# Kernel optimization log

Measured on AMD Instinct MI355X. Metric: run time of the kernel, lower is better.

The kernel has to match this reference:

```python
import jax, jax.numpy as jnp
import numpy as np

B, F0, F1, E, C = 256, 39, 39, 16, 1  # batch, feature_nums[0], feature_nums[1], emb_size, w_channels
_ROWS, _COLS = np.tril_indices(F1, k=-1)  # strict lower triangle of (F1, F0); row-major order matches masked_select
I = _ROWS.shape[0]  # interaction_num = 741
BN_EPS = 1e-5


def setup_inputs() -> dict:
    key = jax.random.key(0)
    k1, k2, k3 = jax.random.split(key, 3)
    xi = jax.random.normal(k1, (B, F0, E), dtype=jnp.float32)
    xj = jax.random.normal(k2, (B, F1, E), dtype=jnp.float32)
    # W param is (1,1,C,E,E) in torch; keep the broadcastable core (C,E,E). Xavier-uniform bound.
    bound = float(np.sqrt(6.0 / (E + E)))
    W = jax.random.uniform(k3, (C, E, E), dtype=jnp.float32, minval=-bound, maxval=bound)
    gamma = jnp.ones((I,), dtype=jnp.float32)   # BatchNorm2d weight
    beta = jnp.zeros((I,), dtype=jnp.float32)   # BatchNorm2d bias
    return {"xi": xi, "xj": xj, "W": W, "gamma": gamma, "beta": beta}


def reference(xi, xj, W, gamma, beta):
    rows = jnp.asarray(_ROWS)
    cols = jnp.asarray(_COLS)
    # raw_cross[b,f1,f0,e1,e2] = xj[b,f1,e1] * xi[b,f0,e2]; only keep strict-lower-tri (f1,f0) pairs.
    # Compute triangular pairs directly instead of materializing the full (B,F1,F0,E,E) tensor.
    cross = xj[:, rows, :, None] * xi[:, cols, None, :]  # (B, I, E, E)
    # BatchNorm2d (training-mode batch stats, biased variance) over channels I
    mean = jnp.mean(cross, axis=(0, 2, 3), keepdims=True)            # (1, I, 1, 1)
    var = jnp.mean(jnp.square(cross - mean), axis=(0, 2, 3), keepdims=True)
    normed = (cross - mean) * jax.lax.rsqrt(var + BN_EPS)
    normed = normed * gamma[None, :, None, None] + beta[None, :, None, None]
    # broadcast multiply with W over w_channels, then transpose(1,2)
    out = normed[:, :, None, :, :] * W[None, None, :, :, :]          # (B, I, C, E, E)
    return jnp.transpose(out, (0, 2, 1, 3, 4))                        # (B, C, I, E, E)
```

## Files before the change

kernel.cpp:

```cpp
#include <hip/hip_runtime.h>
#include <math.h>

#define BB 256
#define FF 39
#define EE 16
#define II 741
#define BN_EPS 1e-5f

typedef float vfloat4 __attribute__((ext_vector_type(4)));


__global__ __launch_bounds__(256) void
stats_kernel(const float* __restrict__ xi,
             const float* __restrict__ xj,
             const float* __restrict__ gamma,
             const float* __restrict__ beta,
             float* __restrict__ ws) {
    int wid = (blockIdx.x * blockDim.x + threadIdx.x) >> 6;
    int lane = threadIdx.x & 63;
    if (wid >= II) return;
    int i = wid;
    int r = (int)((1.0f + sqrtf(8.0f * (float)i + 1.0f)) * 0.5f);
    while (r * (r - 1) / 2 > i) --r;
    while ((r + 1) * r / 2 <= i) ++r;
    int c = i - r * (r - 1) / 2;

    float sumS = 0.f, sumQ = 0.f;
#pragma unroll
    for (int b = lane; b < BB; b += 64) {
        const vfloat4* xjr = reinterpret_cast<const vfloat4*>(xj + (b * FF + r) * EE);
        const vfloat4* xic = reinterpret_cast<const vfloat4*>(xi + (b * FF + c) * EE);
        float sj = 0.f, qj = 0.f, si = 0.f, qi = 0.f;
#pragma unroll
        for (int k = 0; k < 4; ++k) {
            vfloat4 vj = xjr[k];
            vfloat4 vi = xic[k];
            sj += vj.x + vj.y + vj.z + vj.w;
            qj += vj.x * vj.x + vj.y * vj.y + vj.z * vj.z + vj.w * vj.w;
            si += vi.x + vi.y + vi.z + vi.w;
            qi += vi.x * vi.x + vi.y * vi.y + vi.z * vi.z + vi.w * vi.w;
        }
        sumS += sj * si;
        sumQ += qj * qi;
    }
#pragma unroll
    for (int off = 32; off > 0; off >>= 1) {
        sumS += __shfl_xor(sumS, off);
        sumQ += __shfl_xor(sumQ, off);
    }
    if (lane == 0) {
        const float invN = 1.0f / (float)(BB * EE * EE);
        float mean = sumS * invN;
        float ex2 = sumQ * invN;
        float var = ex2 - mean * mean;
        float inv_std = 1.0f / sqrtf(var + BN_EPS);
        float a = gamma[i] * inv_std;
        float d = beta[i] - mean * a;
        vfloat4 e;
        e.x = a; e.y = d; e.z = (float)(r * EE); e.w = (float)(c * EE);
        reinterpret_cast<vfloat4*>(ws)[i] = e;
    }
}

#define CPW 8
__global__ __launch_bounds__(256) void
cross_bn_kernel(const float* __restrict__ xi,
                const float* __restrict__ xj,
                const float* __restrict__ W,
                const float* __restrict__ ws,
                float* __restrict__ out) {
    const vfloat4* T = reinterpret_cast<const vfloat4*>(ws);

    int b = blockIdx.y;
    int t = threadIdx.x;
    int l = t & 63;
    int e1 = l >> 2;
    int e2q = l & 3;
    int wv = t >> 6;

    vfloat4 w4 = reinterpret_cast<const vfloat4*>(W)[e1 * 4 + e2q];

    const float* xib = xi + b * FF * EE;
    const float* xjb = xj + b * FF * EE;
    float* outb = out + (size_t)b * II * EE * EE;

    int ibase = blockIdx.x * (4 * CPW) + wv * CPW;

    if (ibase + CPW <= II) {
        vfloat4 tb[CPW];
#pragma unroll
        for (int k = 0; k < CPW; ++k) tb[k] = T[ibase + k];
        float xjs[CPW];
        vfloat4 xi4[CPW];
#pragma unroll
        for (int k = 0; k < CPW; ++k) {
            xjs[k] = xjb[(int)tb[k].z + e1];
            xi4[k] = reinterpret_cast<const vfloat4*>(xib + (int)tb[k].w)[e2q];
        }
#pragma unroll
        for (int k = 0; k < CPW; ++k) {
            vfloat4 o;
            o.x = (xjs[k] * xi4[k].x * tb[k].x + tb[k].y) * w4.x;
            o.y = (xjs[k] * xi4[k].y * tb[k].x + tb[k].y) * w4.y;
            o.z = (xjs[k] * xi4[k].z * tb[k].x + tb[k].y) * w4.z;
            o.w = (xjs[k] * xi4[k].w * tb[k].x + tb[k].y) * w4.w;
            vfloat4* dst = reinterpret_cast<vfloat4*>(outb + (size_t)(ibase + k) * (EE * EE)) + l;
            *dst = o;
        }
    } else {
#pragma unroll
        for (int k = 0; k < CPW; ++k) {
            int i = ibase + k;
            if (i >= II) break;
            vfloat4 tb = T[i];
            float xjs = xjb[(int)tb.z + e1];
            vfloat4 xi4 = reinterpret_cast<const vfloat4*>(xib + (int)tb.w)[e2q];
            vfloat4 o;
            o.x = (xjs * xi4.x * tb.x + tb.y) * w4.x;
            o.y = (xjs * xi4.y * tb.x + tb.y) * w4.y;
            o.z = (xjs * xi4.z * tb.x + tb.y) * w4.z;
            o.w = (xjs * xi4.w * tb.x + tb.y) * w4.w;
            vfloat4* dst = reinterpret_cast<vfloat4*>(outb + (size_t)i * (EE * EE)) + l;
            *dst = o;
        }
    }
}

extern "C" void kernel_launch(void* const* d_in, const int* in_sizes, int n_in,
                              void* d_out, int out_size, void* d_ws, size_t ws_size,
                              hipStream_t stream) {
    const float* xi = (const float*)d_in[0];
    const float* xj = (const float*)d_in[1];
    const float* W = (const float*)d_in[2];
    const float* gamma = (const float*)d_in[3];
    const float* beta = (const float*)d_in[4];
    float* out = (float*)d_out;
    float* ws = (float*)d_ws;

    stats_kernel<<<dim3((II * 64 + 255) / 256), 256, 0, stream>>>(xi, xj, gamma, beta, ws);
    const int CPB = 4 * CPW;
    cross_bn_kernel<<<dim3((II + CPB - 1) / CPB, BB), 256, 0, stream>>>(xi, xj, W, ws, out);
}
```

Measured before the change: 45.28 us.

## Process several batches per block and use constant offset table

Each block of the main kernel now handles four batch rows, so the per-channel scale/shift and offsets are loaded once and reused across those rows, and the grid shrinks by four. The (row, col) index decode moves to a compile-time constant-memory table of packed offsets, which also lets the stats kernel skip its sqrt-based index recovery and shrinks the workspace entries to two floats. Fewer blocks means less parallelism and more sequential stores per wave on a kernel that is mostly bound by output writes.

Result: faster. 43.14 us (-4.7%).

```diff
diff --git a/kernel.cpp b/kernel.cpp
--- a/kernel.cpp
+++ b/kernel.cpp
@@ -6,8 +6,24 @@
 #define EE 16
 #define II 741
 #define BN_EPS 1e-5f
+#define CPW 8
+#define NB 4
 
 typedef float vfloat4 __attribute__((ext_vector_type(4)));
+typedef float vfloat2 __attribute__((ext_vector_type(2)));
+
+struct OffTab { unsigned int v[II]; };
+static constexpr OffTab make_off() {
+    OffTab t{};
+    int i = 0;
+    for (int r = 1; r < FF; ++r)
+        for (int c = 0; c < r; ++c) {
+            t.v[i] = ((unsigned)(r * EE) << 16) | (unsigned)(c * EE);
+            ++i;
+        }
+    return t;
+}
+__constant__ OffTab g_off = make_off();
 
 
 __global__ __launch_bounds__(256) void
@@ -20,16 +36,15 @@
     int lane = threadIdx.x & 63;
     if (wid >= II) return;
     int i = wid;
-    int r = (int)((1.0f + sqrtf(8.0f * (float)i + 1.0f)) * 0.5f);
-    while (r * (r - 1) / 2 > i) --r;
-    while ((r + 1) * r / 2 <= i) ++r;
-    int c = i - r * (r - 1) / 2;
+    unsigned o = g_off.v[i];
+    int joff = (int)(o >> 16);
+    int coff = (int)(o & 0xffffu);
 
     float sumS = 0.f, sumQ = 0.f;
 #pragma unroll
     for (int b = lane; b < BB; b += 64) {
-        const vfloat4* xjr = reinterpret_cast<const vfloat4*>(xj + (b * FF + r) * EE);
-        const vfloat4* xic = reinterpret_cast<const vfloat4*>(xi + (b * FF + c) * EE);
+        const vfloat4* xjr = reinterpret_cast<const vfloat4*>(xj + b * FF * EE + joff);
+        const vfloat4* xic = reinterpret_cast<const vfloat4*>(xi + b * FF * EE + coff);
         float sj = 0.f, qj = 0.f, si = 0.f, qi = 0.f;
 #pragma unroll
         for (int k = 0; k < 4; ++k) {
@@ -56,22 +71,20 @@
         float inv_std = 1.0f / sqrtf(var + BN_EPS);
         float a = gamma[i] * inv_std;
         float d = beta[i] - mean * a;
-        vfloat4 e;
-        e.x = a; e.y = d; e.z = (float)(r * EE); e.w = (float)(c * EE);
-        reinterpret_cast<vfloat4*>(ws)[i] = e;
+        vfloat2 e;
+        e.x = a; e.y = d;
+        reinterpret_cast<vfloat2*>(ws)[i] = e;
     }
 }
 
-#define CPW 8
 __global__ __launch_bounds__(256) void
 cross_bn_kernel(const float* __restrict__ xi,
                 const float* __restrict__ xj,
                 const float* __restrict__ W,
                 const float* __restrict__ ws,
                 float* __restrict__ out) {
-    const vfloat4* T = reinterpret_cast<const vfloat4*>(ws);
+    const vfloat2* T2 = reinterpret_cast<const vfloat2*>(ws);
 
-    int b = blockIdx.y;
     int t = threadIdx.x;
     int l = t & 63;
     int e1 = l >> 2;
@@ -80,48 +93,66 @@
 
     vfloat4 w4 = reinterpret_cast<const vfloat4*>(W)[e1 * 4 + e2q];
 
-    const float* xib = xi + b * FF * EE;
-    const float* xjb = xj + b * FF * EE;
-    float* outb = out + (size_t)b * II * EE * EE;
-
-    int ibase = blockIdx.x * (4 * CPW) + wv * CPW;
+    int ibase = __builtin_amdgcn_readfirstlane(blockIdx.x * (4 * CPW) + wv * CPW);
+    int b0 = blockIdx.y * NB;
 
     if (ibase + CPW <= II) {
-        vfloat4 tb[CPW];
-#pragma unroll
-        for (int k = 0; k < CPW; ++k) tb[k] = T[ibase + k];
-        float xjs[CPW];
-        vfloat4 xi4[CPW];
+        int joff[CPW], coff[CPW];
+        float a[CPW], d[CPW];
 #pragma unroll
         for (int k = 0; k < CPW; ++k) {
-            xjs[k] = xjb[(int)tb[k].z + e1];
-            xi4[k] = reinterpret_cast<const vfloat4*>(xib + (int)tb[k].w)[e2q];
+            unsigned o = g_off.v[ibase + k];
+            joff[k] = (int)(o >> 16);
+            coff[k] = (int)(o & 0xffffu);
+            vfloat2 ad = T2[ibase + k];
+            a[k] = ad.x; d[k] = ad.y;
         }
 #pragma unroll
-        for (int k = 0; k < CPW; ++k) {
-            vfloat4 o;
-            o.x = (xjs[k] * xi4[k].x * tb[k].x + tb[k].y) * w4.x;
-            o.y = (xjs[k] * xi4[k].y * tb[k].x + tb[k].y) * w4.y;
-            o.z = (xjs[k] * xi4[k].z * tb[k].x + tb[k].y) * w4.z;
-            o.w = (xjs[k] * xi4[k].w * tb[k].x + tb[k].y) * w4.w;
-            vfloat4* dst = reinterpret_cast<vfloat4*>(outb + (size_t)(ibase + k) * (EE * EE)) + l;
-            *dst = o;
+        for (int bb = 0; bb < NB; ++bb) {
+            int b = b0 + bb;
+            const float* xib = xi + b * FF * EE;
+            const float* xjb = xj + b * FF * EE;
+            float* outb = out + (size_t)b * (II * EE * EE) + (size_t)ibase * (EE * EE);
+            float xjs[CPW];
+            vfloat4 xi4[CPW];
+#pragma unroll
+            for (int k = 0; k < CPW; ++k) {
+                xjs[k] = xjb[joff[k] + e1];
+                xi4[k] = reinterpret_cast<const vfloat4*>(xib + coff[k])[e2q];
+            }
+#pragma unroll
+            for (int k = 0; k < CPW; ++k) {
+                vfloat4 o4;
+                o4.x = (xjs[k] * xi4[k].x * a[k] + d[k]) * w4.x;
+                o4.y = (xjs[k] * xi4[k].y * a[k] + d[k]) * w4.y;
+                o4.z = (xjs[k] * xi4[k].z * a[k] + d[k]) * w4.z;
+                o4.w = (xjs[k] * xi4[k].w * a[k] + d[k]) * w4.w;
+                reinterpret_cast<vfloat4*>(outb + k * (EE * EE))[l] = o4;
+            }
         }
     } else {
 #pragma unroll
-        for (int k = 0; k < CPW; ++k) {
-            int i = ibase + k;
-            if (i >= II) break;
-            vfloat4 tb = T[i];
-            float xjs = xjb[(int)tb.z + e1];
-            vfloat4 xi4 = reinterpret_cast<const vfloat4*>(xib + (int)tb.w)[e2q];
-            vfloat4 o;
-            o.x = (xjs * xi4.x * tb.x + tb.y) * w4.x;
-            o.y = (xjs * xi4.y * tb.x + tb.y) * w4.y;
-            o.z = (xjs * xi4.z * tb.x + tb.y) * w4.z;
-            o.w = (xjs * xi4.w * tb.x + tb.y) * w4.w;
-            vfloat4* dst = reinterpret_cast<vfloat4*>(outb + (size_t)i * (EE * EE)) + l;
-            *dst = o;
+        for (int bb = 0; bb < NB; ++bb) {
+            int b = b0 + bb;
+            const float* xib = xi + b * FF * EE;
+            const float* xjb = xj + b * FF * EE;
+            float* outb = out + (size_t)b * (II * EE * EE);
+            for (int k = 0; k < CPW; ++k) {
+                int i = ibase + k;
+                if (i >= II) break;
+                unsigned o = g_off.v[i];
+                int joff = (int)(o >> 16);
+                int coff = (int)(o & 0xffffu);
+                vfloat2 ad = T2[i];
+                float xjs = xjb[joff + e1];
+                vfloat4 xi4 = reinterpret_cast<const vfloat4*>(xib + coff)[e2q];
+                vfloat4 o4;
+                o4.x = (xjs * xi4.x * ad.x + ad.y) * w4.x;
+                o4.y = (xjs * xi4.y * ad.x + ad.y) * w4.y;
+                o4.z = (xjs * xi4.z * ad.x + ad.y) * w4.z;
+                o4.w = (xjs * xi4.w * ad.x + ad.y) * w4.w;
+                reinterpret_cast<vfloat4*>(outb + (size_t)i * (EE * EE))[l] = o4;
+            }
         }
     }
 }
@@ -139,5 +170,5 @@
 
     stats_kernel<<<dim3((II * 64 + 255) / 256), 256, 0, stream>>>(xi, xj, gamma, beta, ws);
     const int CPB = 4 * CPW;
-    cross_bn_kernel<<<dim3((II + CPB - 1) / CPB, BB), 256, 0, stream>>>(xi, xj, W, ws, out);
+    cross_bn_kernel<<<dim3((II + CPB - 1) / CPB, BB / NB), 256, 0, stream>>>(xi, xj, W, ws, out);
 }
```
